# Kernel tuning notes

Hardware: AMD Instinct MI355X
Metric: run time of the kernel (lower is better)

Reference implementation:

```python
import jax, jax.numpy as jnp
import numpy as np

POOL = (7, 7, 3)          # (py, px, pz) pool_size
N_LEVELS = 4              # pyramid_levels = [0,1,2,3]


def setup_inputs() -> dict:
    key = jax.random.key(0)
    ks = jax.random.split(key, 8)
    B, C = 2, 48
    shapes = [(96, 96, 48), (48, 48, 24), (24, 24, 12), (12, 12, 6)]
    fm = {f"fmap{i}": jax.random.normal(ks[i], (B, C) + shapes[i], jnp.float32)
          for i in range(N_LEVELS)}
    N = 1200
    ctr = jax.random.uniform(ks[4], (N, 3), minval=0.15, maxval=0.85)
    sz = jax.random.uniform(ks[5], (N, 3), minval=0.05, maxval=0.5)
    lo = jnp.clip(ctr - sz / 2, 0.0, 1.0)
    hi = jnp.clip(ctr + sz / 2, 0.0, 1.0)
    bix = jax.random.randint(ks[6], (N,), 0, B).astype(jnp.float32)
    # rois: (N, (y1, x1, y2, x2, z1, z2, batch_ix)) normalized coords
    rois = jnp.stack([lo[:, 0], lo[:, 1], hi[:, 0], hi[:, 1],
                      lo[:, 2], hi[:, 2], bix], axis=1)
    return {**fm, "rois": rois}


def _roi_align_3d(fmap, boxes, bix, pool):
    """fmap: (B,C,Y,X,Z); boxes: (N,6) in fmap pixel coords; bix: (N,) int32.
    Trilinear roi_align, sampling one point per bin center. Returns (N,C,py,px,pz)."""
    B, C, Y, X, Z = fmap.shape
    py, px, pz = pool
    N = boxes.shape[0]
    y1, x1, y2, x2, z1, z2 = (boxes[:, i] for i in range(6))

    def centers(a, b, n):
        binsz = (b - a) / n
        return a[:, None] + (jnp.arange(n, dtype=boxes.dtype) + 0.5) * binsz[:, None]

    ys = centers(y1, y2, py)  # (N, py)
    xs = centers(x1, x2, px)  # (N, px)
    zs = centers(z1, z2, pz)  # (N, pz)
    S = py * px * pz
    yy = jnp.broadcast_to(ys[:, :, None, None], (N, py, px, pz)).reshape(N, S)
    xx = jnp.broadcast_to(xs[:, None, :, None], (N, py, px, pz)).reshape(N, S)
    zz = jnp.broadcast_to(zs[:, None, None, :], (N, py, px, pz)).reshape(N, S)

    valid = ((yy > -1.0) & (yy < Y) & (xx > -1.0) & (xx < X)
             & (zz > -1.0) & (zz < Z))
    yc = jnp.clip(yy, 0.0, Y - 1)
    xc = jnp.clip(xx, 0.0, X - 1)
    zc = jnp.clip(zz, 0.0, Z - 1)

    y0 = jnp.floor(yc).astype(jnp.int32); y1i = jnp.minimum(y0 + 1, Y - 1)
    x0 = jnp.floor(xc).astype(jnp.int32); x1i = jnp.minimum(x0 + 1, X - 1)
    z0 = jnp.floor(zc).astype(jnp.int32); z1i = jnp.minimum(z0 + 1, Z - 1)
    ly = yc - y0; hy = 1.0 - ly
    lx = xc - x0; hx = 1.0 - lx
    lz = zc - z0; hz = 1.0 - lz

    fm = jnp.transpose(fmap, (0, 2, 3, 4, 1))  # (B,Y,X,Z,C)
    b = jnp.broadcast_to(bix[:, None], (N, S))

    def g(yi, xi, zi):
        return fm[b, yi, xi, zi]  # (N,S,C)

    val = (g(y0, x0, z0) * (hy * hx * hz)[..., None]
           + g(y0, x0, z1i) * (hy * hx * lz)[..., None]
           + g(y0, x1i, z0) * (hy * lx * hz)[..., None]
           + g(y0, x1i, z1i) * (hy * lx * lz)[..., None]
           + g(y1i, x0, z0) * (ly * hx * hz)[..., None]
           + g(y1i, x0, z1i) * (ly * hx * lz)[..., None]
           + g(y1i, x1i, z0) * (ly * lx * hz)[..., None]
           + g(y1i, x1i, z1i) * (ly * lx * lz)[..., None])
    val = jnp.where(valid[..., None], val, 0.0)
    return jnp.transpose(val.reshape(N, py, px, pz, C), (0, 4, 1, 2, 3))


def reference(fmap0, fmap1, fmap2, fmap3, rois):
    fmaps = [fmap0, fmap1, fmap2, fmap3]
    boxes = rois[:, :6]
    bix = rois[:, 6].astype(jnp.int32)
    h = boxes[:, 2] - boxes[:, 0]
    w = boxes[:, 3] - boxes[:, 1]
    # roi_level = round(4 + log2(sqrt(h*w))).clamp(levels[0], levels[-1])
    roi_level = jnp.clip(jnp.round(4.0 + 0.5 * jnp.log2(h * w)),
                         0, N_LEVELS - 1).astype(jnp.int32)
    out = jnp.zeros((rois.shape[0], fmap0.shape[1]) + POOL, rois.dtype)
    for lvl, fmap in enumerate(fmaps):
        Y, X, Z = fmap.shape[2:]
        scale = jnp.array([Y, X, Y, X, Z, Z], dtype=rois.dtype)
        pooled = _roi_align_3d(fmap, boxes * scale, bix, POOL)
        sel = (roi_level == lvl)[:, None, None, None, None]
        out = out + jnp.where(sel, pooled, 0.0)
    # Equivalent to the torch code's per-level index_select + concat + sort
    # reassembly: output is in original roi order.
    return out
```

## Files before the change

### kernel.cpp

```cpp
#include <hip/hip_runtime.h>

#define POOL_Y 7
#define POOL_X 7
#define POOL_Z 3
#define S_BINS (POOL_Y * POOL_X * POOL_Z)
#define C_CH   48
#define PER_ROI (C_CH * S_BINS)

__global__ __launch_bounds__(256) void roialign3d_kernel(
    const float* __restrict__ f0, const float* __restrict__ f1,
    const float* __restrict__ f2, const float* __restrict__ f3,
    const float* __restrict__ rois, float* __restrict__ out, int total)
{
    int idx = blockIdx.x * blockDim.x + threadIdx.x;
    if (idx >= total) return;

    int n   = idx / PER_ROI;
    int rem = idx - n * PER_ROI;
    int c   = rem / S_BINS;
    int s   = rem - c * S_BINS;
    int ybin = s / (POOL_X * POOL_Z);
    int rs   = s - ybin * (POOL_X * POOL_Z);
    int xbin = rs / POOL_Z;
    int zbin = rs - xbin * POOL_Z;

    const float* r = rois + n * 7;
    float by1 = r[0], bx1 = r[1], by2 = r[2], bx2 = r[3], bz1 = r[4], bz2 = r[5];
    int b = (int)r[6];

    float h = by2 - by1, w = bx2 - bx1;
    float lv = rintf(4.0f + 0.5f * log2f(h * w));
    lv = fminf(fmaxf(lv, 0.0f), 3.0f);
    int level = (int)lv;

    const float* fm; int Y, X, Z;
    switch (level) {
        case 0: fm = f0; Y = 96; X = 96; Z = 48; break;
        case 1: fm = f1; Y = 48; X = 48; Z = 24; break;
        case 2: fm = f2; Y = 24; X = 24; Z = 12; break;
        default: fm = f3; Y = 12; X = 12; Z = 6;  break;
    }

    float fy1 = by1 * Y, fy2 = by2 * Y;
    float fx1 = bx1 * X, fx2 = bx2 * X;
    float fz1 = bz1 * Z, fz2 = bz2 * Z;

    float yy = fy1 + (ybin + 0.5f) * (fy2 - fy1) * (1.0f / POOL_Y);
    float xx = fx1 + (xbin + 0.5f) * (fx2 - fx1) * (1.0f / POOL_X);
    float zz = fz1 + (zbin + 0.5f) * (fz2 - fz1) * (1.0f / POOL_Z);

    bool valid = (yy > -1.0f) && (yy < (float)Y) &&
                 (xx > -1.0f) && (xx < (float)X) &&
                 (zz > -1.0f) && (zz < (float)Z);

    float yc = fminf(fmaxf(yy, 0.0f), (float)(Y - 1));
    float xc = fminf(fmaxf(xx, 0.0f), (float)(X - 1));
    float zc = fminf(fmaxf(zz, 0.0f), (float)(Z - 1));

    int y0 = (int)floorf(yc);
    int x0 = (int)floorf(xc);
    int z0 = (int)floorf(zc);
    int y1i = min(y0 + 1, Y - 1);
    int x1i = min(x0 + 1, X - 1);

    float ly = yc - (float)y0, lx = xc - (float)x0, lz = zc - (float)z0;
    float hy = 1.0f - ly,      hx = 1.0f - lx,      hz = 1.0f - lz;

    int  zb    = min(z0, Z - 2);
    bool shift = (zb != z0);
    float wlo  = shift ? 0.0f : hz;
    float whi  = shift ? 1.0f : lz;

    const float* base = fm + ((size_t)b * C_CH + c) * (size_t)Y * X * Z;

    const float2 v00 = *(const float2*)(base + (size_t)(y0  * X + x0 ) * Z + zb);
    const float2 v01 = *(const float2*)(base + (size_t)(y0  * X + x1i) * Z + zb);
    const float2 v10 = *(const float2*)(base + (size_t)(y1i * X + x0 ) * Z + zb);
    const float2 v11 = *(const float2*)(base + (size_t)(y1i * X + x1i) * Z + zb);

    float w00 = hy * hx, w01 = hy * lx, w10 = ly * hx, w11 = ly * lx;
    float lo = w00 * v00.x + w01 * v01.x + w10 * v10.x + w11 * v11.x;
    float hi = w00 * v00.y + w01 * v01.y + w10 * v10.y + w11 * v11.y;
    float val = wlo * lo + whi * hi;

    __builtin_nontemporal_store(valid ? val : 0.0f, &out[idx]);
}

extern "C" void kernel_launch(void* const* d_in, const int* in_sizes, int n_in,
                              void* d_out, int out_size, void* d_ws, size_t ws_size,
                              hipStream_t stream) {
    const float* f0   = (const float*)d_in[0];
    const float* f1   = (const float*)d_in[1];
    const float* f2   = (const float*)d_in[2];
    const float* f3   = (const float*)d_in[3];
    const float* rois = (const float*)d_in[4];
    float* out = (float*)d_out;

    int total = out_size;
    int block = 256;
    int grid  = (total + block - 1) / block;
    roialign3d_kernel<<<grid, block, 0, stream>>>(f0, f1, f2, f3, rois, out, total);
}
```

Baseline: 44.41 us.

## Use one block per ROI and precompute bin offsets and weights in shared memory

Launches one 256-thread block per ROI instead of one thread per output element. The first 147 threads compute each bin's level selection, trilinear offsets and weights once and store them in LDS. All threads then loop over the 7056 channel-bin outputs, reusing the shared tables. This removes redundant per-element ROI math and integer divisions, at the cost of a barrier, fewer total blocks (1200) and a serial setup phase per block.

```diff
diff --git a/kernel.cpp b/kernel.cpp
--- a/kernel.cpp
+++ b/kernel.cpp
@@ -1,89 +1,122 @@
 #include <hip/hip_runtime.h>
 
-#define POOL_Y 7
-#define POOL_X 7
-#define POOL_Z 3
-#define S_BINS (POOL_Y * POOL_X * POOL_Z)
+#define PY 7
+#define PX 7
+#define PZ 3
+#define S_BINS 147
 #define C_CH   48
-#define PER_ROI (C_CH * S_BINS)
+#define PER_ROI 7056
 
 __global__ __launch_bounds__(256) void roialign3d_kernel(
     const float* __restrict__ f0, const float* __restrict__ f1,
     const float* __restrict__ f2, const float* __restrict__ f3,
-    const float* __restrict__ rois, float* __restrict__ out, int total)
+    const float* __restrict__ rois, float* __restrict__ out)
 {
-    int idx = blockIdx.x * blockDim.x + threadIdx.x;
-    if (idx >= total) return;
+    __shared__ int   s_o00[S_BINS], s_o01[S_BINS], s_o10[S_BINS], s_o11[S_BINS];
+    __shared__ float s_w00[S_BINS], s_w01[S_BINS], s_w10[S_BINS], s_w11[S_BINS];
+    __shared__ float s_wlo[S_BINS], s_whi[S_BINS];
+    __shared__ const float* s_base;
+    __shared__ int s_plane;
 
-    int n   = idx / PER_ROI;
-    int rem = idx - n * PER_ROI;
-    int c   = rem / S_BINS;
-    int s   = rem - c * S_BINS;
-    int ybin = s / (POOL_X * POOL_Z);
-    int rs   = s - ybin * (POOL_X * POOL_Z);
-    int xbin = rs / POOL_Z;
-    int zbin = rs - xbin * POOL_Z;
+    const int n   = blockIdx.x;
+    const int tid = threadIdx.x;
+    const float* r = rois + n * 7;
 
-    const float* r = rois + n * 7;
-    float by1 = r[0], bx1 = r[1], by2 = r[2], bx2 = r[3], bz1 = r[4], bz2 = r[5];
-    int b = (int)r[6];
+    if (tid < S_BINS) {
+        float by1 = r[0], bx1 = r[1], by2 = r[2], bx2 = r[3], bz1 = r[4], bz2 = r[5];
+        int b = (int)r[6];
 
-    float h = by2 - by1, w = bx2 - bx1;
-    float lv = rintf(4.0f + 0.5f * log2f(h * w));
-    lv = fminf(fmaxf(lv, 0.0f), 3.0f);
-    int level = (int)lv;
+        float h = by2 - by1, w = bx2 - bx1;
+        float lv = rintf(4.0f + 0.5f * log2f(h * w));
+        lv = fminf(fmaxf(lv, 0.0f), 3.0f);
+        int level = (int)lv;
 
-    const float* fm; int Y, X, Z;
-    switch (level) {
-        case 0: fm = f0; Y = 96; X = 96; Z = 48; break;
-        case 1: fm = f1; Y = 48; X = 48; Z = 24; break;
-        case 2: fm = f2; Y = 24; X = 24; Z = 12; break;
-        default: fm = f3; Y = 12; X = 12; Z = 6;  break;
+        const float* fm; int Y, X, Z;
+        switch (level) {
+            case 0: fm = f0; Y = 96; X = 96; Z = 48; break;
+            case 1: fm = f1; Y = 48; X = 48; Z = 24; break;
+            case 2: fm = f2; Y = 24; X = 24; Z = 12; break;
+            default: fm = f3; Y = 12; X = 12; Z = 6;  break;
+        }
+
+        int s    = tid;
+        int ybin = s / (PX * PZ);
+        int rs   = s - ybin * (PX * PZ);
+        int xbin = rs / PZ;
+        int zbin = rs - xbin * PZ;
+
+        float fy1 = by1 * Y, fy2 = by2 * Y;
+        float fx1 = bx1 * X, fx2 = bx2 * X;
+        float fz1 = bz1 * Z, fz2 = bz2 * Z;
+
+        float yy = fy1 + (ybin + 0.5f) * (fy2 - fy1) * (1.0f / PY);
+        float xx = fx1 + (xbin + 0.5f) * (fx2 - fx1) * (1.0f / PX);
+        float zz = fz1 + (zbin + 0.5f) * (fz2 - fz1) * (1.0f / PZ);
+
+        bool valid = (yy > -1.0f) && (yy < (float)Y) &&
+                     (xx > -1.0f) && (xx < (float)X) &&
+                     (zz > -1.0f) && (zz < (float)Z);
+
+        float yc = fminf(fmaxf(yy, 0.0f), (float)(Y - 1));
+        float xc = fminf(fmaxf(xx, 0.0f), (float)(X - 1));
+        float zc = fminf(fmaxf(zz, 0.0f), (float)(Z - 1));
+
+        int y0 = (int)floorf(yc);
+        int x0 = (int)floorf(xc);
+        int z0 = (int)floorf(zc);
+        int y1i = min(y0 + 1, Y - 1);
+        int x1i = min(x0 + 1, X - 1);
+
+        float ly = yc - (float)y0, lx = xc - (float)x0, lz = zc - (float)z0;
+        float hy = 1.0f - ly,      hx = 1.0f - lx,      hz = 1.0f - lz;
+
+        int  zb    = min(z0, Z - 2);
+        bool shift = (zb != z0);
+        float wlo  = shift ? 0.0f : hz;
+        float whi  = shift ? 1.0f : lz;
+        if (!valid) { wlo = 0.0f; whi = 0.0f; }
+
+        s_o00[s] = (y0  * X + x0 ) * Z + zb;
+        s_o01[s] = (y0  * X + x1i) * Z + zb;
+        s_o10[s] = (y1i * X + x0 ) * Z + zb;
+        s_o11[s] = (y1i * X + x1i) * Z + zb;
+        s_w00[s] = hy * hx;
+        s_w01[s] = hy * lx;
+        s_w10[s] = ly * hx;
+        s_w11[s] = ly * lx;
+        s_wlo[s] = wlo;
+        s_whi[s] = whi;
+
+        if (s == 0) {
+            int plane = Y * X * Z;
+            s_base  = fm + (size_t)b * C_CH * plane;
+            s_plane = plane;
+        }
     }
+    __syncthreads();
 
-    float fy1 = by1 * Y, fy2 = by2 * Y;
-    float fx1 = bx1 * X, fx2 = bx2 * X;
-    float fz1 = bz1 * Z, fz2 = bz2 * Z;
+    const float* base = s_base;
+    const int plane   = s_plane;
+    float* outroi = out + (size_t)n * PER_ROI;
 
-    float yy = fy1 + (ybin + 0.5f) * (fy2 - fy1) * (1.0f / POOL_Y);
-    float xx = fx1 + (xbin + 0.5f) * (fx2 - fx1) * (1.0f / POOL_X);
-    float zz = fz1 + (zbin + 0.5f) * (fz2 - fz1) * (1.0f / POOL_Z);
+    #pragma unroll 2
+    for (int oi = tid; oi < PER_ROI; oi += 256) {
+        unsigned c = (unsigned)oi / 147u;
+        unsigned s = (unsigned)oi - c * 147u;
+        const float* p = base + (unsigned)plane * c;
 
-    bool valid = (yy > -1.0f) && (yy < (float)Y) &&
-                 (xx > -1.0f) && (xx < (float)X) &&
-                 (zz > -1.0f) && (zz < (float)Z);
+        float2 v00 = *(const float2*)(p + s_o00[s]);
+        float2 v01 = *(const float2*)(p + s_o01[s]);
+        float2 v10 = *(const float2*)(p + s_o10[s]);
+        float2 v11 = *(const float2*)(p + s_o11[s]);
 
-    float yc = fminf(fmaxf(yy, 0.0f), (float)(Y - 1));
-    float xc = fminf(fmaxf(xx, 0.0f), (float)(X - 1));
-    float zc = fminf(fmaxf(zz, 0.0f), (float)(Z - 1));
+        float w00 = s_w00[s], w01 = s_w01[s], w10 = s_w10[s], w11 = s_w11[s];
+        float lo = w00 * v00.x + w01 * v01.x + w10 * v10.x + w11 * v11.x;
+        float hi = w00 * v00.y + w01 * v01.y + w10 * v10.y + w11 * v11.y;
+        float val = s_wlo[s] * lo + s_whi[s] * hi;
 
-    int y0 = (int)floorf(yc);
-    int x0 = (int)floorf(xc);
-    int z0 = (int)floorf(zc);
-    int y1i = min(y0 + 1, Y - 1);
-    int x1i = min(x0 + 1, X - 1);
-
-    float ly = yc - (float)y0, lx = xc - (float)x0, lz = zc - (float)z0;
-    float hy = 1.0f - ly,      hx = 1.0f - lx,      hz = 1.0f - lz;
-
-    int  zb    = min(z0, Z - 2);
-    bool shift = (zb != z0);
-    float wlo  = shift ? 0.0f : hz;
-    float whi  = shift ? 1.0f : lz;
-
-    const float* base = fm + ((size_t)b * C_CH + c) * (size_t)Y * X * Z;
-
-    const float2 v00 = *(const float2*)(base + (size_t)(y0  * X + x0 ) * Z + zb);
-    const float2 v01 = *(const float2*)(base + (size_t)(y0  * X + x1i) * Z + zb);
-    const float2 v10 = *(const float2*)(base + (size_t)(y1i * X + x0 ) * Z + zb);
-    const float2 v11 = *(const float2*)(base + (size_t)(y1i * X + x1i) * Z + zb);
-
-    float w00 = hy * hx, w01 = hy * lx, w10 = ly * hx, w11 = ly * lx;
-    float lo = w00 * v00.x + w01 * v01.x + w10 * v10.x + w11 * v11.x;
-    float hi = w00 * v00.y + w01 * v01.y + w10 * v10.y + w11 * v11.y;
-    float val = wlo * lo + whi * hi;
-
-    __builtin_nontemporal_store(valid ? val : 0.0f, &out[idx]);
+        __builtin_nontemporal_store(val, &outroi[oi]);
+    }
 }
 
 extern "C" void kernel_launch(void* const* d_in, const int* in_sizes, int n_in,
@@ -96,8 +129,6 @@
     const float* rois = (const float*)d_in[4];
     float* out = (float*)d_out;
 
-    int total = out_size;
-    int block = 256;
-    int grid  = (total + block - 1) / block;
-    roialign3d_kernel<<<grid, block, 0, stream>>>(f0, f1, f2, f3, rois, out, total);
+    int n_rois = out_size / PER_ROI;
+    roialign3d_kernel<<<n_rois, 256, 0, stream>>>(f0, f1, f2, f3, rois, out);
 }
```

Result: faster. 36.22 us (-18.4%).

## Compute each bin once per thread and loop over channels

Applied to the files above, without the earlier changes.

Each thread now handles one (roi, bin) pair and loops over all 48 channels. It computes the ROI decode, level selection, coordinates and trilinear weights once and reuses them across channels instead of once per output element. The grid shrinks by a factor of 48, which cuts total work and integer division overhead but lowers parallelism to about 176K threads. Stores remain coalesced across bins within a channel.

```diff
diff --git a/kernel.cpp b/kernel.cpp
--- a/kernel.cpp
+++ b/kernel.cpp
@@ -1,28 +1,22 @@
 #include <hip/hip_runtime.h>
 
-#define POOL_Y 7
-#define POOL_X 7
-#define POOL_Z 3
-#define S_BINS (POOL_Y * POOL_X * POOL_Z)
+#define PY 7
+#define PX 7
+#define PZ 3
+#define S_BINS 147
 #define C_CH   48
-#define PER_ROI (C_CH * S_BINS)
+#define PER_ROI 7056
 
 __global__ __launch_bounds__(256) void roialign3d_kernel(
     const float* __restrict__ f0, const float* __restrict__ f1,
     const float* __restrict__ f2, const float* __restrict__ f3,
-    const float* __restrict__ rois, float* __restrict__ out, int total)
+    const float* __restrict__ rois, float* __restrict__ out, int total_bins)
 {
-    int idx = blockIdx.x * blockDim.x + threadIdx.x;
-    if (idx >= total) return;
+    int t = blockIdx.x * blockDim.x + threadIdx.x;
+    if (t >= total_bins) return;
 
-    int n   = idx / PER_ROI;
-    int rem = idx - n * PER_ROI;
-    int c   = rem / S_BINS;
-    int s   = rem - c * S_BINS;
-    int ybin = s / (POOL_X * POOL_Z);
-    int rs   = s - ybin * (POOL_X * POOL_Z);
-    int xbin = rs / POOL_Z;
-    int zbin = rs - xbin * POOL_Z;
+    unsigned n = (unsigned)t / S_BINS;
+    unsigned s = (unsigned)t - n * S_BINS;
 
     const float* r = rois + n * 7;
     float by1 = r[0], bx1 = r[1], by2 = r[2], bx2 = r[3], bz1 = r[4], bz2 = r[5];
@@ -41,13 +35,18 @@
         default: fm = f3; Y = 12; X = 12; Z = 6;  break;
     }
 
+    int ybin = s / (PX * PZ);
+    int rs   = s - ybin * (PX * PZ);
+    int xbin = rs / PZ;
+    int zbin = rs - xbin * PZ;
+
     float fy1 = by1 * Y, fy2 = by2 * Y;
     float fx1 = bx1 * X, fx2 = bx2 * X;
     float fz1 = bz1 * Z, fz2 = bz2 * Z;
 
-    float yy = fy1 + (ybin + 0.5f) * (fy2 - fy1) * (1.0f / POOL_Y);
-    float xx = fx1 + (xbin + 0.5f) * (fx2 - fx1) * (1.0f / POOL_X);
-    float zz = fz1 + (zbin + 0.5f) * (fz2 - fz1) * (1.0f / POOL_Z);
+    float yy = fy1 + (ybin + 0.5f) * (fy2 - fy1) * (1.0f / PY);
+    float xx = fx1 + (xbin + 0.5f) * (fx2 - fx1) * (1.0f / PX);
+    float zz = fz1 + (zbin + 0.5f) * (fz2 - fz1) * (1.0f / PZ);
 
     bool valid = (yy > -1.0f) && (yy < (float)Y) &&
                  (xx > -1.0f) && (xx < (float)X) &&
@@ -70,20 +69,36 @@
     bool shift = (zb != z0);
     float wlo  = shift ? 0.0f : hz;
     float whi  = shift ? 1.0f : lz;
-
-    const float* base = fm + ((size_t)b * C_CH + c) * (size_t)Y * X * Z;
-
-    const float2 v00 = *(const float2*)(base + (size_t)(y0  * X + x0 ) * Z + zb);
-    const float2 v01 = *(const float2*)(base + (size_t)(y0  * X + x1i) * Z + zb);
-    const float2 v10 = *(const float2*)(base + (size_t)(y1i * X + x0 ) * Z + zb);
-    const float2 v11 = *(const float2*)(base + (size_t)(y1i * X + x1i) * Z + zb);
+    if (!valid) { wlo = 0.0f; whi = 0.0f; }
 
     float w00 = hy * hx, w01 = hy * lx, w10 = ly * hx, w11 = ly * lx;
-    float lo = w00 * v00.x + w01 * v01.x + w10 * v10.x + w11 * v11.x;
-    float hi = w00 * v00.y + w01 * v01.y + w10 * v10.y + w11 * v11.y;
-    float val = wlo * lo + whi * hi;
 
-    __builtin_nontemporal_store(valid ? val : 0.0f, &out[idx]);
+    const int plane = Y * X * Z;
+    const float* base = fm + (size_t)b * C_CH * plane;
+
+    const float* p00 = base + (y0  * X + x0 ) * Z + zb;
+    const float* p01 = base + (y0  * X + x1i) * Z + zb;
+    const float* p10 = base + (y1i * X + x0 ) * Z + zb;
+    const float* p11 = base + (y1i * X + x1i) * Z + zb;
+
+    float* op = out + (size_t)n * PER_ROI + s;
+
+    #pragma unroll 4
+    for (int c = 0; c < C_CH; ++c) {
+        float2 v00 = *(const float2*)p00;
+        float2 v01 = *(const float2*)p01;
+        float2 v10 = *(const float2*)p10;
+        float2 v11 = *(const float2*)p11;
+
+        float lo = w00 * v00.x + w01 * v01.x + w10 * v10.x + w11 * v11.x;
+        float hi = w00 * v00.y + w01 * v01.y + w10 * v10.y + w11 * v11.y;
+        float val = wlo * lo + whi * hi;
+
+        __builtin_nontemporal_store(val, op);
+
+        p00 += plane; p01 += plane; p10 += plane; p11 += plane;
+        op += S_BINS;
+    }
 }
 
 extern "C" void kernel_launch(void* const* d_in, const int* in_sizes, int n_in,
@@ -96,8 +111,9 @@
     const float* rois = (const float*)d_in[4];
     float* out = (float*)d_out;
 
-    int total = out_size;
+    int n_rois = out_size / PER_ROI;
+    int total_bins = n_rois * S_BINS;
     int block = 256;
-    int grid  = (total + block - 1) / block;
-    roialign3d_kernel<<<grid, block, 0, stream>>>(f0, f1, f2, f3, rois, out, total);
+    int grid  = (total_bins + block - 1) / block;
+    roialign3d_kernel<<<grid, block, 0, stream>>>(f0, f1, f2, f3, rois, out, total_bins);
 }
```

New measurement: 35.79 us (median of 2 runs). 19.4% less time.
